# Kernel tuning notes

Hardware: AMD Instinct MI355X
Metric: run time of the kernel (lower is better)

Reference implementation:

```python
import jax, jax.numpy as jnp
import numpy as np

N = 16384          # nodes
E = 262144         # edges (before self-loops)
FIN_N, FIN_E = 768, 64
F, FE = 256, 128   # node/edge channels
H, C = 8, 32       # heads, per-head dim (H*C == F)
L = 2              # num GATv2 modules
NEG_SLOPE = 0.2


def layer_norm(x, g, b, eps=1e-5):
    mu = jnp.mean(x, axis=-1, keepdims=True)
    var = jnp.mean((x - mu) ** 2, axis=-1, keepdims=True)
    return (x - mu) * jax.lax.rsqrt(var + eps) * g + b


def segment_softmax(logits, seg, n):
    # logits: [Et, H], seg: [Et] destination node ids
    m = jax.ops.segment_max(logits, seg, num_segments=n)
    m = jnp.where(jnp.isfinite(m), m, 0.0)
    e = jnp.exp(logits - m[seg])
    s = jax.ops.segment_sum(e, seg, num_segments=n)
    return e / (s[seg] + 1e-16)


def setup_inputs() -> dict:
    key = jax.random.key(0)
    ks = jax.random.split(key, 20)
    inp = {
        "node_feats": jax.random.normal(ks[0], (N, FIN_N), jnp.float32),
        "edge_index": jax.random.randint(ks[1], (2, E), 0, N, dtype=jnp.int32),
        "edge_attr": jax.random.normal(ks[2], (E, FIN_E), jnp.float32),
        # input projections (bias=False)
        "init_node_w": jax.random.normal(ks[3], (F, FIN_N), jnp.float32) * 0.02,
        "init_edge_w": jax.random.normal(ks[4], (FE, FIN_E), jnp.float32) * 0.02,
        # per-layer GATv2 params, stacked on leading layer dim L
        "lin_l_w": jax.random.normal(ks[5], (L, H * C, F), jnp.float32) * 0.05,
        "lin_l_b": jnp.zeros((L, H * C), jnp.float32),
        "lin_r_w": jax.random.normal(ks[6], (L, H * C, F), jnp.float32) * 0.05,
        "lin_r_b": jnp.zeros((L, H * C), jnp.float32),
        "lin_edge_w": jax.random.normal(ks[7], (L, H * C, FE), jnp.float32) * 0.05,
        "att": jax.random.normal(ks[8], (L, H, C), jnp.float32) * 0.05,
        "gat_bias": jnp.zeros((L, H * C), jnp.float32),
        # block params
        "ln1_g": jnp.ones((L, F), jnp.float32), "ln1_b": jnp.zeros((L, F), jnp.float32),
        "mlp_w1": jax.random.normal(ks[9], (L, 2 * F, F), jnp.float32) * 0.05,
        "mlp_w2": jax.random.normal(ks[10], (L, F, 2 * F), jnp.float32) * 0.05,
        "ln2_g": jnp.ones((L, F), jnp.float32), "ln2_b": jnp.zeros((L, F), jnp.float32),
    }
    return inp


def _gatv2_module(x, src, dst, e_emb, p, l, n):
    # e_emb: [Et, H, C] already projected edge embeddings (incl. self-loops)
    x_l = (x @ p["lin_l_w"][l].T + p["lin_l_b"][l]).reshape(n, H, C)
    x_r = (x @ p["lin_r_w"][l].T + p["lin_r_b"][l]).reshape(n, H, C)
    m = x_l[src] + x_r[dst] + e_emb                    # [Et, H, C]
    g = jnp.where(m >= 0, m, NEG_SLOPE * m)            # leaky_relu(0.2)
    logits = jnp.einsum('ehc,hc->eh', g, p["att"][l])
    alpha = segment_softmax(logits, dst, n)            # [Et, H]
    out = jax.ops.segment_sum(alpha[:, :, None] * x_l[src], dst, num_segments=n)
    out = out.reshape(n, H * C) + p["gat_bias"][l]
    # residual -> LN -> MLP -> residual -> LN  (dropout=0, eval mode)
    h = layer_norm(x + out, p["ln1_g"][l], p["ln1_b"][l])
    y = jax.nn.gelu(h @ p["mlp_w1"][l].T, approximate=False) @ p["mlp_w2"][l].T
    return layer_norm(h + y, p["ln2_g"][l], p["ln2_b"][l])


def reference(node_feats, edge_index, edge_attr, init_node_w, init_edge_w,
              lin_l_w, lin_l_b, lin_r_w, lin_r_b, lin_edge_w, att, gat_bias,
              ln1_g, ln1_b, mlp_w1, mlp_w2, ln2_g, ln2_b):
    p = dict(lin_l_w=lin_l_w, lin_l_b=lin_l_b, lin_r_w=lin_r_w, lin_r_b=lin_r_b,
             lin_edge_w=lin_edge_w, att=att, gat_bias=gat_bias, ln1_g=ln1_g,
             ln1_b=ln1_b, mlp_w1=mlp_w1, mlp_w2=mlp_w2, ln2_g=ln2_g, ln2_b=ln2_b)
    x = node_feats @ init_node_w.T                     # [N, F]
    ea = edge_attr @ init_edge_w.T                     # [E, FE]
    src, dst = edge_index[0], edge_index[1]
    # add self loops with fill_value='mean' (mean of incoming edge_attr per node)
    cnt = jax.ops.segment_sum(jnp.ones((E,), ea.dtype), dst, num_segments=N)
    loop_attr = jax.ops.segment_sum(ea, dst, num_segments=N) / jnp.maximum(cnt, 1.0)[:, None]
    ea_all = jnp.concatenate([ea, loop_attr], axis=0)  # [E+N, FE]
    ar = jnp.arange(N, dtype=src.dtype)
    src_all = jnp.concatenate([src, ar])
    dst_all = jnp.concatenate([dst, ar])
    for l in range(L):
        e_emb = (ea_all @ lin_edge_w[l].T).reshape(-1, H, C)
        x = _gatv2_module(x, src_all, dst_all, e_emb, p, l, N)
    return x
```

## Files before the change

### kernel.cpp

```cpp
#include <hip/hip_runtime.h>

typedef unsigned short u16;
typedef __attribute__((ext_vector_type(8))) short s8v;
typedef __attribute__((ext_vector_type(4))) float f4v;

#define NN 16384
#define EE 262144
#define ET (EE + NN)
#define NTILES (ET / 64)

__device__ __forceinline__ float bfu(u16 h){ return __uint_as_float((unsigned)h << 16); }
__device__ __forceinline__ u16 f2bf(float f){
  unsigned u = __float_as_uint(f);
  unsigned r = u + 0x7FFFu + ((u >> 16) & 1u);
  return (u16)(r >> 16);
}
__device__ __forceinline__ float ldf(const void* p, size_t i, int isbf){
  return isbf ? bfu(((const u16*)p)[i]) : ((const float*)p)[i];
}
__device__ __forceinline__ float gelu_f(float x){ return 0.5f*x*(1.0f+erff(x*0.7071067811865475f)); }

__device__ __forceinline__ uint4 load8bf(const void* p, size_t eoff, int isbf){
  if (isbf) return *(const uint4*)((const u16*)p + eoff);
  const float* f = (const float*)p + eoff;
  uint4 r;
  r.x = (unsigned)f2bf(f[0]) | ((unsigned)f2bf(f[1])<<16);
  r.y = (unsigned)f2bf(f[2]) | ((unsigned)f2bf(f[3])<<16);
  r.z = (unsigned)f2bf(f[4]) | ((unsigned)f2bf(f[5])<<16);
  r.w = (unsigned)f2bf(f[6]) | ((unsigned)f2bf(f[7])<<16);
  return r;
}

__global__ void k_detect(const void* nf, int* flag)
{
  int t = threadIdx.x;
  const float* f = (const float*)nf;
  int cnt = 0;
  for (int i = t; i < 4096; i += 256) {
    float a = fabsf(f[i]);
    if (a > 1e-5f && a < 100.0f) cnt++;
  }
  __shared__ int s[256];
  s[t] = cnt; __syncthreads();
  for (int st = 128; st > 0; st >>= 1) { if (t < st) s[t] += s[t+st]; __syncthreads(); }
  if (t == 0) *flag = (s[0] < 2048) ? 1 : 0;
}

template<int ACT, int CFMT>
__global__ __launch_bounds__(256)
void mfma_gemm(const void* __restrict__ A, int a_fmt,
               const void* __restrict__ B1, size_t b1off,
               const void* __restrict__ B2, size_t b2off, int nsplit,
               const void* __restrict__ bias1, const void* __restrict__ bias2,
               size_t bioff, int has_bias,
               void* __restrict__ C, int M, int N, int K,
               const int* __restrict__ dflag)
{
  int isbf = *dflag;
  int af = (a_fmt == 2) ? isbf : a_fmt;
  __shared__ u16 As[128*40];
  __shared__ u16 Bs[128*40];
  int bm = blockIdx.y*128, bn = blockIdx.x*128;
  int t = threadIdx.x;
  int w = t>>6, lane = t&63, l4 = lane&15, quad = lane>>4;
  int wm = w>>1, wn = w&1;
  f4v zero = {0.f,0.f,0.f,0.f};
  f4v acc[4][4];
  #pragma unroll
  for (int i=0;i<4;i++)
    #pragma unroll
    for (int j=0;j<4;j++) acc[i][j] = zero;

  for (int k0 = 0; k0 < K; k0 += 32) {
    __syncthreads();
    #pragma unroll
    for (int it = 0; it < 2; ++it) {
      int sid = t + it*256;
      int row = sid >> 2, sk = sid & 3;
      *(uint4*)&As[row*40 + sk*8] = load8bf(A, (size_t)(bm+row)*K + k0 + sk*8, af);
      int col = bn + row;
      uint4 vb;
      if (col < nsplit) vb = load8bf(B1, b1off + (size_t)col*K + k0 + sk*8, isbf);
      else              vb = load8bf(B2, b2off + (size_t)(col-nsplit)*K + k0 + sk*8, isbf);
      *(uint4*)&Bs[row*40 + sk*8] = vb;
    }
    __syncthreads();
    s8v a[4], b[4];
    #pragma unroll
    for (int i=0;i<4;i++) a[i] = *(const s8v*)&As[(wm*64 + i*16 + l4)*40 + quad*8];
    #pragma unroll
    for (int j=0;j<4;j++) b[j] = *(const s8v*)&Bs[(wn*64 + j*16 + l4)*40 + quad*8];
    #pragma unroll
    for (int i=0;i<4;i++)
      #pragma unroll
      for (int j=0;j<4;j++)
        acc[i][j] = __builtin_amdgcn_mfma_f32_16x16x32_bf16(a[i], b[j], acc[i][j], 0,0,0);
  }
  #pragma unroll
  for (int i=0;i<4;i++)
    #pragma unroll
    for (int j=0;j<4;j++) {
      int col = bn + wn*64 + j*16 + l4;
      float bv = 0.f;
      if (has_bias) bv = (col < nsplit) ? ldf(bias1, bioff + col, isbf)
                                        : ldf(bias2, bioff + col - nsplit, isbf);
      #pragma unroll
      for (int r=0;r<4;r++) {
        int row = bm + wm*64 + i*16 + quad*4 + r;
        float v = acc[i][j][r] + bv;
        if (ACT==1) v = gelu_f(v);
        if (CFMT==1) ((u16*)C)[(size_t)row*N + col] = f2bf(v);
        else         ((float*)C)[(size_t)row*N + col] = v;
      }
    }
}

__global__ void k_count(const int* __restrict__ dst, int* __restrict__ deg)
{
  int e = blockIdx.x*256 + threadIdx.x;
  if (e >= ET) return;
  int d = (e < EE) ? dst[e] : (e - EE);
  atomicAdd(&deg[d], 1);
}

__global__ void k_scan(const int* __restrict__ deg, int* __restrict__ rowstart)
{
  __shared__ int csum[256];
  int t = threadIdx.x;
  int s = 0;
  for (int i=0;i<64;i++) s += deg[t*64+i];
  csum[t] = s;
  __syncthreads();
  if (t == 0) {
    int r = 0;
    for (int i=0;i<256;i++){ int v = csum[i]; csum[i] = r; r += v; }
    rowstart[NN] = r;
  }
  __syncthreads();
  int b = csum[t];
  for (int i=0;i<64;i++){ rowstart[t*64+i] = b; b += deg[t*64+i]; }
}

__global__ void k_scatter(const int* __restrict__ dst, const int* __restrict__ rowstart,
                          int* __restrict__ fill, int* __restrict__ csr)
{
  int e = blockIdx.x*256 + threadIdx.x;
  if (e >= ET) return;
  int d = (e < EE) ? dst[e] : (e - EE);
  int pos = rowstart[d] + atomicAdd(&fill[d], 1);
  csr[pos] = e;
}

__global__ void k_loopmean(const int* __restrict__ csr, const int* __restrict__ rowstart,
                           const void* __restrict__ edge_attr, u16* __restrict__ loopmean,
                           const int* __restrict__ dflag)
{
  int isbf = *dflag;
  int n = blockIdx.x, j = threadIdx.x;
  int s = rowstart[n], e1 = rowstart[n+1];
  float sum = 0.f; int cnt = 0;
  for (int p = s; p < e1; ++p) {
    int eid = csr[p];
    if (eid < EE) { sum += ldf(edge_attr, (size_t)eid*64 + j, isbf); cnt++; }
  }
  loopmean[(size_t)n*64 + j] = f2bf(sum / (float)max(cnt, 1));
}

__global__ void k_wc(const void* __restrict__ We, const void* __restrict__ iew,
                     u16* __restrict__ Wcb, const int* __restrict__ dflag)
{
  int isbf = *dflag;
  int idx = blockIdx.x*256 + threadIdx.x;
  int j = idx & 63, c = (idx >> 6) & 255, l = idx >> 14;
  float s = 0.f;
  for (int k=0;k<128;k++) s += ldf(We, ((size_t)l*256 + c)*128 + k, isbf) * ldf(iew, (size_t)k*64 + j, isbf);
  Wcb[idx] = f2bf(s);
}

__global__ __launch_bounds__(256)
void k_elogits(const int* __restrict__ src, const int* __restrict__ dst,
               const u16* __restrict__ Wcb, const u16* __restrict__ xlr,
               const void* __restrict__ edge_attr, const u16* __restrict__ loopmean,
               const void* __restrict__ att, size_t att_off,
               float* __restrict__ logits, const int* __restrict__ dflag)
{
  int isbf = *dflag;
  __shared__ u16 WcF[32*64*8];
  __shared__ u16 attr_s[64*72];
  __shared__ float satt[256];
  __shared__ int ssrc[64], sdst[64];

  int t = threadIdx.x;
  int w = t>>6, lane = t&63, l4 = lane&15, quad = lane>>4;

  satt[t] = ldf(att, att_off + t, isbf);
  #pragma unroll
  for (int f = 0; f < 8; ++f) {
    int fr = w + f*4;
    int i = fr >> 1, ks = fr & 1;
    *(uint4*)&WcF[(fr*64 + lane)*8] = *(const uint4*)&Wcb[(size_t)(16*i + l4)*64 + ks*32 + quad*8];
  }

  f4v zero = {0.f,0.f,0.f,0.f};
  for (int tile = blockIdx.x; tile < NTILES; tile += gridDim.x) {
    int e0 = tile*64;
    __syncthreads();
    if (t < 64) {
      int e = e0 + t;
      ssrc[t] = (e < EE) ? src[e] : (e - EE);
      sdst[t] = (e < EE) ? dst[e] : (e - EE);
    }
    {
      int er = t >> 2, part = t & 3;
      int e = e0 + er;
      uint4 v0, v1;
      if (e < EE) {
        v0 = load8bf(edge_attr, (size_t)e*64 + part*16,     isbf);
        v1 = load8bf(edge_attr, (size_t)e*64 + part*16 + 8, isbf);
      } else {
        v0 = *(const uint4*)&loopmean[(size_t)(e-EE)*64 + part*16];
        v1 = *(const uint4*)&loopmean[(size_t)(e-EE)*64 + part*16 + 8];
      }
      *(uint4*)&attr_s[er*72 + part*16]     = v0;
      *(uint4*)&attr_s[er*72 + part*16 + 8] = v1;
    }
    __syncthreads();

    s8v b0 = *(const s8v*)&attr_s[(w*16 + l4)*72 + quad*8];
    s8v b1 = *(const s8v*)&attr_s[(w*16 + l4)*72 + 32 + quad*8];
    f4v acc[16];
    #pragma unroll
    for (int i=0;i<16;++i){
      s8v a0 = *(const s8v*)&WcF[((2*i  )*64 + lane)*8];
      s8v a1 = *(const s8v*)&WcF[((2*i+1)*64 + lane)*8];
      acc[i] = __builtin_amdgcn_mfma_f32_16x16x32_bf16(a0, b0, zero, 0,0,0);
      acc[i] = __builtin_amdgcn_mfma_f32_16x16x32_bf16(a1, b1, acc[i], 0,0,0);
    }

    int me = w*16 + l4;
    int sn = ssrc[me], dn = sdst[me];
    float ph[8] = {0.f,0.f,0.f,0.f,0.f,0.f,0.f,0.f};
    #pragma unroll
    for (int i=0;i<16;++i){
      uint2 xlv = *(const uint2*)&xlr[(size_t)sn*512 +       i*16 + quad*4];
      uint2 xrv = *(const uint2*)&xlr[(size_t)dn*512 + 256 + i*16 + quad*4];
      float4 av = *(const float4*)&satt[i*16 + quad*4];
      float m0 = acc[i][0] + bfu((u16)(xlv.x & 0xffff)) + bfu((u16)(xrv.x & 0xffff));
      float m1 = acc[i][1] + bfu((u16)(xlv.x >> 16))    + bfu((u16)(xrv.x >> 16));
      float m2 = acc[i][2] + bfu((u16)(xlv.y & 0xffff)) + bfu((u16)(xrv.y & 0xffff));
      float m3 = acc[i][3] + bfu((u16)(xlv.y >> 16))    + bfu((u16)(xrv.y >> 16));
      float g0 = fmaxf(m0, 0.2f*m0), g1 = fmaxf(m1, 0.2f*m1);
      float g2 = fmaxf(m2, 0.2f*m2), g3 = fmaxf(m3, 0.2f*m3);
      ph[i>>1] += av.x*g0 + av.y*g1 + av.z*g2 + av.w*g3;
    }
    #pragma unroll
    for (int h=0;h<8;++h){
      ph[h] += __shfl_xor(ph[h], 16);
      ph[h] += __shfl_xor(ph[h], 32);
    }
    if (quad == 0){
      float4 lo = {ph[0], ph[1], ph[2], ph[3]};
      float4 hi = {ph[4], ph[5], ph[6], ph[7]};
      *(float4*)&logits[(size_t)(e0 + me)*8]     = lo;
      *(float4*)&logits[(size_t)(e0 + me)*8 + 4] = hi;
    }
  }
}

__global__ __launch_bounds__(256)
void k_aggln(const int* __restrict__ csr, const int* __restrict__ rowstart, const int* __restrict__ src,
             const float* __restrict__ logits, const u16* __restrict__ xlr, const float* __restrict__ xbuf,
             const void* __restrict__ gat_bias, const void* __restrict__ ln1g, const void* __restrict__ ln1b,
             size_t poff, float* __restrict__ hbuf, const int* __restrict__ dflag)
{
  int isbf = *dflag;
  int lane = threadIdx.x & 63, wid = threadIdx.x >> 6;
  int n = blockIdx.x*4 + wid;
  int s = rowstart[n], deg = rowstart[n+1] - s;
  int myh = lane >> 3;
  float mrun = -3.0e38f, lrun = 0.f;
  float a0=0.f, a1=0.f, a2=0.f, a3=0.f;

  for (int c0 = 0; c0 < deg; c0 += 64) {
    int idx = s + c0 + lane; if (idx >= ET) idx = ET-1;
    int ev = csr[idx];
    int sv = (ev < EE) ? src[ev] : (ev - EE);
    int lim = min(64, deg - c0);
    for (int j = 0; j < lim; ++j) {
      int eid = __shfl(ev, j);
      int sn  = __shfl(sv, j);
      float lg = logits[(size_t)eid*8 + myh];
      uint2 xv = *(const uint2*)&xlr[(size_t)sn*512 + 4*lane];
      float mn = fmaxf(mrun, lg);
      float sc = __expf(mrun - mn);
      float wv = __expf(lg - mn);
      mrun = mn;
      lrun = lrun*sc + wv;
      a0 = a0*sc + wv*bfu((u16)(xv.x & 0xffff));
      a1 = a1*sc + wv*bfu((u16)(xv.x >> 16));
      a2 = a2*sc + wv*bfu((u16)(xv.y & 0xffff));
      a3 = a3*sc + wv*bfu((u16)(xv.y >> 16));
    }
  }
  float inv = 1.f/(lrun + 1e-16f);
  int c = 4*lane;
  float4 res = *(const float4*)&xbuf[(size_t)n*256 + c];
  float o0 = a0*inv + ldf(gat_bias, poff+c+0, isbf) + res.x;
  float o1 = a1*inv + ldf(gat_bias, poff+c+1, isbf) + res.y;
  float o2 = a2*inv + ldf(gat_bias, poff+c+2, isbf) + res.z;
  float o3 = a3*inv + ldf(gat_bias, poff+c+3, isbf) + res.w;

  float v = o0+o1+o2+o3;
  #pragma unroll
  for (int off=1; off<64; off<<=1) v += __shfl_xor(v, off);
  float mu = v * (1.f/256.f);
  float d0=o0-mu, d1=o1-mu, d2=o2-mu, d3=o3-mu;
  float v2 = d0*d0+d1*d1+d2*d2+d3*d3;
  #pragma unroll
  for (int off=1; off<64; off<<=1) v2 += __shfl_xor(v2, off);
  float wn = rsqrtf(v2*(1.f/256.f) + 1e-5f);
  float4 outv;
  outv.x = d0*wn*ldf(ln1g, poff+c+0, isbf) + ldf(ln1b, poff+c+0, isbf);
  outv.y = d1*wn*ldf(ln1g, poff+c+1, isbf) + ldf(ln1b, poff+c+1, isbf);
  outv.z = d2*wn*ldf(ln1g, poff+c+2, isbf) + ldf(ln1b, poff+c+2, isbf);
  outv.w = d3*wn*ldf(ln1g, poff+c+3, isbf) + ldf(ln1b, poff+c+3, isbf);
  *(float4*)&hbuf[(size_t)n*256 + c] = outv;
}

__global__ __launch_bounds__(256)
void k_ln_add(const float* __restrict__ a, const u16* __restrict__ b2,
              const void* __restrict__ gg, const void* __restrict__ bb, size_t poff,
              float* __restrict__ out, const int* __restrict__ dflag)
{
  int isbf = *dflag;
  int n = blockIdx.x, t = threadIdx.x;
  __shared__ float r[256];
  float x = a[(size_t)n*256 + t] + bfu(b2[(size_t)n*256 + t]);
  r[t] = x; __syncthreads();
  for (int st = 128; st > 0; st >>= 1) { if (t < st) r[t] += r[t+st]; __syncthreads(); }
  float mu = r[0] * (1.f/256.f);
  __syncthreads();
  float d = x - mu;
  r[t] = d*d; __syncthreads();
  for (int st = 128; st > 0; st >>= 1) { if (t < st) r[t] += r[t+st]; __syncthreads(); }
  float var = r[0] * (1.f/256.f);
  out[(size_t)n*256 + t] = d * rsqrtf(var + 1e-5f) * ldf(gg, poff + t, isbf) + ldf(bb, poff + t, isbf);
}

__global__ void k_out(const float* __restrict__ x, void* __restrict__ out, const int* __restrict__ dflag)
{
  int isbf = *dflag;
  int i = blockIdx.x*256 + threadIdx.x;
  if (isbf) ((u16*)out)[i] = f2bf(x[i]);
  else      ((float*)out)[i] = x[i];
}

extern "C" void kernel_launch(void* const* d_in, const int* in_sizes, int n_in,
                              void* d_out, int out_size, void* d_ws, size_t ws_size,
                              hipStream_t stream)
{
  const void* node_feats = d_in[0];
  const int*  edge_index = (const int*)d_in[1];
  const void* edge_attr  = d_in[2];
  const void* init_node_w= d_in[3];
  const void* init_edge_w= d_in[4];
  const void* lin_l_w    = d_in[5];
  const void* lin_l_b    = d_in[6];
  const void* lin_r_w    = d_in[7];
  const void* lin_r_b    = d_in[8];
  const void* lin_edge_w = d_in[9];
  const void* att        = d_in[10];
  const void* gat_bias   = d_in[11];
  const void* ln1_g      = d_in[12];
  const void* ln1_b      = d_in[13];
  const void* mlp_w1     = d_in[14];
  const void* mlp_w2     = d_in[15];
  const void* ln2_g      = d_in[16];
  const void* ln2_b      = d_in[17];

  const int* srcp = edge_index;
  const int* dstp = edge_index + EE;

  char* p = (char*)d_ws;
  auto alloc = [&](size_t bytes) { void* r = (void*)p; p += (bytes + 255) & ~(size_t)255; return r; };
  int*   dflag   = (int*)alloc(256);
  int*   deg     = (int*)alloc((size_t)NN*4);
  int*   rowstart= (int*)alloc((size_t)(NN+1)*4);
  int*   fill    = (int*)alloc((size_t)NN*4);
  int*   csr     = (int*)alloc((size_t)ET*4);
  u16*   Wcb     = (u16*)alloc((size_t)2*256*64*2);
  u16*   loopmean= (u16*)alloc((size_t)NN*64*2);
  float* logits  = (float*)alloc((size_t)ET*8*4);
  float* xbuf    = (float*)alloc((size_t)NN*256*4);
  float* hbuf    = (float*)alloc((size_t)NN*256*4);
  u16*   xlr     = (u16*)alloc((size_t)NN*512*2);
  u16*   ymid    = xlr;
  u16*   y2      = (u16*)d_out;

  hipMemsetAsync(deg,  0, (size_t)NN*4, stream);
  hipMemsetAsync(fill, 0, (size_t)NN*4, stream);

  k_detect <<<1, 256, 0, stream>>>(node_feats, dflag);

  k_count  <<<(ET+255)/256, 256, 0, stream>>>(dstp, deg);
  k_scan   <<<1, 256, 0, stream>>>(deg, rowstart);
  k_scatter<<<(ET+255)/256, 256, 0, stream>>>(dstp, rowstart, fill, csr);
  k_loopmean<<<NN, 64, 0, stream>>>(csr, rowstart, edge_attr, loopmean, dflag);
  k_wc     <<<128, 256, 0, stream>>>(lin_edge_w, init_edge_w, Wcb, dflag);

  mfma_gemm<0,0><<<dim3(2,128), 256, 0, stream>>>(node_feats, 2, init_node_w, 0, init_node_w, 0, 1<<29,
                                                  nullptr, nullptr, 0, 0, xbuf, NN, 256, 768, dflag);

  for (int l = 0; l < 2; ++l) {
    size_t wo = (size_t)l*256*256;
    size_t bo = (size_t)l*256;
    mfma_gemm<0,1><<<dim3(4,128), 256, 0, stream>>>(xbuf, 0, lin_l_w, wo, lin_r_w, wo, 256,
                                                    lin_l_b, lin_r_b, bo, 1, xlr, NN, 512, 256, dflag);
    k_elogits<<<768, 256, 0, stream>>>(srcp, dstp, Wcb + (size_t)l*256*64, xlr,
                                       edge_attr, loopmean, att, (size_t)l*256, logits, dflag);
    k_aggln<<<NN/4, 256, 0, stream>>>(csr, rowstart, srcp, logits, xlr, xbuf,
                                      gat_bias, ln1_g, ln1_b, bo, hbuf, dflag);
    mfma_gemm<1,1><<<dim3(4,128), 256, 0, stream>>>(hbuf, 0, mlp_w1, (size_t)l*512*256, mlp_w1, 0, 1<<29,
                                                    nullptr, nullptr, 0, 0, ymid, NN, 512, 256, dflag);
    mfma_gemm<0,1><<<dim3(2,128), 256, 0, stream>>>(ymid, 1, mlp_w2, (size_t)l*256*512, mlp_w2, 0, 1<<29,
                                                    nullptr, nullptr, 0, 0, y2, NN, 256, 512, dflag);
    k_ln_add<<<NN, 256, 0, stream>>>(hbuf, y2, ln2_g, ln2_b, bo, xbuf, dflag);
  }

  k_out<<<(NN*256)/256, 256, 0, stream>>>(xbuf, d_out, dflag);
}
```

Before: 779.6 us.

## Process edges in destination-sorted CSR order to make logits accesses contiguous

```diff
diff --git a/kernel.cpp b/kernel.cpp
--- a/kernel.cpp
+++ b/kernel.cpp
@@ -141,14 +141,19 @@
   for (int i=0;i<64;i++){ rowstart[t*64+i] = b; b += deg[t*64+i]; }
 }
 
-__global__ void k_scatter(const int* __restrict__ dst, const int* __restrict__ rowstart,
-                          int* __restrict__ fill, int* __restrict__ csr)
+__global__ void k_scatter(const int* __restrict__ src, const int* __restrict__ dst,
+                          const int* __restrict__ rowstart,
+                          int* __restrict__ fill, int* __restrict__ csr,
+                          int* __restrict__ srcc, int* __restrict__ dstc)
 {
   int e = blockIdx.x*256 + threadIdx.x;
   if (e >= ET) return;
-  int d = (e < EE) ? dst[e] : (e - EE);
+  int d  = (e < EE) ? dst[e] : (e - EE);
+  int sv = (e < EE) ? src[e] : (e - EE);
   int pos = rowstart[d] + atomicAdd(&fill[d], 1);
-  csr[pos] = e;
+  csr[pos]  = e;
+  srcc[pos] = sv;
+  dstc[pos] = d;
 }
 
 __global__ void k_loopmean(const int* __restrict__ csr, const int* __restrict__ rowstart,
@@ -178,7 +183,7 @@
 }
 
 __global__ __launch_bounds__(256)
-void k_elogits(const int* __restrict__ src, const int* __restrict__ dst,
+void k_elogits(const int* __restrict__ csr, const int* __restrict__ srcc, const int* __restrict__ dstc,
                const u16* __restrict__ Wcb, const u16* __restrict__ xlr,
                const void* __restrict__ edge_attr, const u16* __restrict__ loopmean,
                const void* __restrict__ att, size_t att_off,
@@ -206,20 +211,19 @@
     int e0 = tile*64;
     __syncthreads();
     if (t < 64) {
-      int e = e0 + t;
-      ssrc[t] = (e < EE) ? src[e] : (e - EE);
-      sdst[t] = (e < EE) ? dst[e] : (e - EE);
+      ssrc[t] = srcc[e0 + t];
+      sdst[t] = dstc[e0 + t];
     }
     {
       int er = t >> 2, part = t & 3;
-      int e = e0 + er;
+      int eid = csr[e0 + er];
       uint4 v0, v1;
-      if (e < EE) {
-        v0 = load8bf(edge_attr, (size_t)e*64 + part*16,     isbf);
-        v1 = load8bf(edge_attr, (size_t)e*64 + part*16 + 8, isbf);
+      if (eid < EE) {
+        v0 = load8bf(edge_attr, (size_t)eid*64 + part*16,     isbf);
+        v1 = load8bf(edge_attr, (size_t)eid*64 + part*16 + 8, isbf);
       } else {
-        v0 = *(const uint4*)&loopmean[(size_t)(e-EE)*64 + part*16];
-        v1 = *(const uint4*)&loopmean[(size_t)(e-EE)*64 + part*16 + 8];
+        v0 = *(const uint4*)&loopmean[(size_t)(eid-EE)*64 + part*16];
+        v1 = *(const uint4*)&loopmean[(size_t)(eid-EE)*64 + part*16 + 8];
       }
       *(uint4*)&attr_s[er*72 + part*16]     = v0;
       *(uint4*)&attr_s[er*72 + part*16 + 8] = v1;
@@ -268,7 +272,7 @@
 }
 
 __global__ __launch_bounds__(256)
-void k_aggln(const int* __restrict__ csr, const int* __restrict__ rowstart, const int* __restrict__ src,
+void k_aggln(const int* __restrict__ srcc, const int* __restrict__ rowstart,
              const float* __restrict__ logits, const u16* __restrict__ xlr, const float* __restrict__ xbuf,
              const void* __restrict__ gat_bias, const void* __restrict__ ln1g, const void* __restrict__ ln1b,
              size_t poff, float* __restrict__ hbuf, const int* __restrict__ dflag)
@@ -283,13 +287,12 @@
 
   for (int c0 = 0; c0 < deg; c0 += 64) {
     int idx = s + c0 + lane; if (idx >= ET) idx = ET-1;
-    int ev = csr[idx];
-    int sv = (ev < EE) ? src[ev] : (ev - EE);
+    int sv = srcc[idx];
     int lim = min(64, deg - c0);
+    size_t lbase = (size_t)(s + c0)*8 + myh;
     for (int j = 0; j < lim; ++j) {
-      int eid = __shfl(ev, j);
       int sn  = __shfl(sv, j);
-      float lg = logits[(size_t)eid*8 + myh];
+      float lg = logits[lbase + (size_t)j*8];
       uint2 xv = *(const uint2*)&xlr[(size_t)sn*512 + 4*lane];
       float mn = fmaxf(mrun, lg);
       float sc = __expf(mrun - mn);
@@ -388,6 +391,8 @@
   int*   rowstart= (int*)alloc((size_t)(NN+1)*4);
   int*   fill    = (int*)alloc((size_t)NN*4);
   int*   csr     = (int*)alloc((size_t)ET*4);
+  int*   srcc    = (int*)alloc((size_t)ET*4);
+  int*   dstc    = (int*)alloc((size_t)ET*4);
   u16*   Wcb     = (u16*)alloc((size_t)2*256*64*2);
   u16*   loopmean= (u16*)alloc((size_t)NN*64*2);
   float* logits  = (float*)alloc((size_t)ET*8*4);
@@ -404,7 +409,7 @@
 
   k_count  <<<(ET+255)/256, 256, 0, stream>>>(dstp, deg);
   k_scan   <<<1, 256, 0, stream>>>(deg, rowstart);
-  k_scatter<<<(ET+255)/256, 256, 0, stream>>>(dstp, rowstart, fill, csr);
+  k_scatter<<<(ET+255)/256, 256, 0, stream>>>(srcp, dstp, rowstart, fill, csr, srcc, dstc);
   k_loopmean<<<NN, 64, 0, stream>>>(csr, rowstart, edge_attr, loopmean, dflag);
   k_wc     <<<128, 256, 0, stream>>>(lin_edge_w, init_edge_w, Wcb, dflag);
 
@@ -416,9 +421,9 @@
     size_t bo = (size_t)l*256;
     mfma_gemm<0,1><<<dim3(4,128), 256, 0, stream>>>(xbuf, 0, lin_l_w, wo, lin_r_w, wo, 256,
                                                     lin_l_b, lin_r_b, bo, 1, xlr, NN, 512, 256, dflag);
-    k_elogits<<<768, 256, 0, stream>>>(srcp, dstp, Wcb + (size_t)l*256*64, xlr,
+    k_elogits<<<768, 256, 0, stream>>>(csr, srcc, dstc, Wcb + (size_t)l*256*64, xlr,
                                        edge_attr, loopmean, att, (size_t)l*256, logits, dflag);
-    k_aggln<<<NN/4, 256, 0, stream>>>(csr, rowstart, srcp, logits, xlr, xbuf,
+    k_aggln<<<NN/4, 256, 0, stream>>>(srcc, rowstart, logits, xlr, xbuf,
                                       gat_bias, ln1_g, ln1_b, bo, hbuf, dflag);
     mfma_gemm<1,1><<<dim3(4,128), 256, 0, stream>>>(hbuf, 0, mlp_w1, (size_t)l*512*256, mlp_w1, 0, 1<<29,
                                                     nullptr, nullptr, 0, 0, ymid, NN, 512, 256, dflag);
```

Measured after the change: 735.3 us. 5.7% less time.
